# Kernel optimization log

Hardware: AMD Instinct MI355X
Metric: run time of the kernel (lower is better)

The kernel has to match this reference:

```python
import jax, jax.numpy as jnp
import numpy as np

OUT = 7          # out_size
SCALE = 0.25     # spatial_scale
SAMPLE = 2       # sample_num (samples per bin edge)
NORI = 8         # nOrientation
TWO_PI = 2.0 * np.pi


def setup_inputs() -> dict:
    key = jax.random.key(0)
    k1, k2, k3, k4, k5 = jax.random.split(key, 5)
    N, C, H, W = 2, 256, 128, 128
    R = 4096
    features = jax.random.normal(k1, (N, C, H, W), dtype=jnp.float32)
    # rois: (batch_idx, cx, cy, w, h, theta) in image coords (image ~512x512)
    bidx = jax.random.randint(k2, (R, 1), 0, N).astype(jnp.float32)
    cxy = jax.random.uniform(k3, (R, 2), minval=32.0, maxval=480.0, dtype=jnp.float32)
    wh = jax.random.uniform(k4, (R, 2), minval=16.0, maxval=256.0, dtype=jnp.float32)
    theta = jax.random.uniform(k5, (R, 1), minval=0.0, maxval=TWO_PI, dtype=jnp.float32)
    rois = jnp.concatenate([bidx, cxy, wh, theta], axis=1)
    return {"features": features, "rois": rois}


def riroi_align(features, rois):
    """Rotation-invariant RoIAlign (ReDet RiRoIAlign) forward.

    features: [N, C, H, W] with C = c_per * NORI, channel layout c*NORI + o.
    rois:     [R, 6] = (batch_idx, cx, cy, w, h, theta).
    returns:  [R, C, OUT, OUT]
    """
    N, C, H, W = features.shape
    c_per = C // NORI
    g = SAMPLE

    def one_roi(roi):
        b = roi[0].astype(jnp.int32)
        cx = roi[1] * SCALE
        cy = roi[2] * SCALE
        rw = jnp.maximum(roi[3] * SCALE, 1.0)
        rh = jnp.maximum(roi[4] * SCALE, 1.0)
        theta = roi[5]
        bin_w = rw / OUT
        bin_h = rh / OUT
        idx = jnp.arange(OUT, dtype=jnp.float32)
        off = (jnp.arange(g, dtype=jnp.float32) + 0.5) / g
        # local (un-rotated) sample coords, roi-centered; P = OUT*g points per axis
        yy = (-rh / 2 + idx[:, None] * bin_h + off[None, :] * bin_h).reshape(-1)
        xx = (-rw / 2 + idx[:, None] * bin_w + off[None, :] * bin_w).reshape(-1)
        c_t, s_t = jnp.cos(theta), jnp.sin(theta)
        x = xx[None, :] * c_t + yy[:, None] * s_t + cx   # [P, P]
        y = yy[:, None] * c_t - xx[None, :] * s_t + cy   # [P, P]

        # bilinear interpolation with RoIAlign border conventions
        valid = (y > -1.0) & (y < H) & (x > -1.0) & (x < W)
        xc = jnp.clip(x, 0.0, None)
        yc = jnp.clip(y, 0.0, None)
        x0 = jnp.floor(xc).astype(jnp.int32)
        y0 = jnp.floor(yc).astype(jnp.int32)
        hx = x0 >= W - 1
        hy = y0 >= H - 1
        x0 = jnp.where(hx, W - 1, x0)
        x1 = jnp.where(hx, W - 1, x0 + 1)
        y0 = jnp.where(hy, H - 1, y0)
        y1 = jnp.where(hy, H - 1, y0 + 1)
        xc = jnp.where(hx, x0.astype(jnp.float32), xc)
        yc = jnp.where(hy, y0.astype(jnp.float32), yc)
        lx = xc - x0
        ly = yc - y0
        wx0 = 1.0 - lx
        wy0 = 1.0 - ly

        def gat(yi, xi):
            return features[b, :, yi, xi]  # [P, P, C]

        val = ((wy0 * wx0)[..., None] * gat(y0, x0)
               + (wy0 * lx)[..., None] * gat(y0, x1)
               + (ly * wx0)[..., None] * gat(y1, x0)
               + (ly * lx)[..., None] * gat(y1, x1))
        val = jnp.where(valid[..., None], val, 0.0)       # [P, P, C]
        val = jnp.moveaxis(val, -1, 0)                    # [C, P, P]
        # average the g x g samples within each output bin
        val = val.reshape(C, OUT, g, OUT, g).mean(axis=(2, 4))  # [C, OUT, OUT]

        # orientation-channel circular rotation with linear interpolation
        ind_f = theta * NORI / TWO_PI
        ind0 = jnp.floor(ind_f)
        l = ind_f - ind0
        ind = ind0.astype(jnp.int32) % NORI
        o = jnp.arange(NORI)
        src = (o - ind) % NORI
        src_p = (src + 1) % NORI
        v = val.reshape(c_per, NORI, OUT, OUT)
        out = (1.0 - l) * v[:, src] + l * v[:, src_p]
        return out.reshape(C, OUT, OUT)

    return jax.vmap(one_roi)(rois)  # [R, C, OUT, OUT]


def reference(features, rois):
    return riroi_align(features, rois)
```

## Files before the change

### kernel.cpp

```cpp
#include <hip/hip_runtime.h>

typedef _Float16 half_t;
typedef int   v2i __attribute__((ext_vector_type(2)));
typedef int   v4i __attribute__((ext_vector_type(4)));
typedef float v4f __attribute__((ext_vector_type(4)));

#define OUTS 7
#define NORI 8
#define NCH  256
#define FH   128
#define FW   128
#define HW   (FH * FW)
#define NSAMP (2 * OUTS * 2 * OUTS)
#define NBIN  (OUTS * OUTS)
#define WBINS 7
#define NBKT  512

struct __align__(32) Geom { int o[4]; float w[4]; };

__global__ __launch_bounds__(256) void transpose_nchw_nhwc_h(
    const float* __restrict__ in, half_t* __restrict__ out) {
  __shared__ float tile[64][65];
  const int b  = blockIdx.z;
  const int p0 = blockIdx.x * 64;
  const int c0 = blockIdx.y * 64;
  const int tx = threadIdx.x & 63;
  const int ty = threadIdx.x >> 6;

  const float* src = in + ((size_t)b * NCH + c0) * HW + p0;
#pragma unroll
  for (int i = 0; i < 16; ++i) {
    int c = ty + i * 4;
    tile[c][tx] = src[(size_t)c * HW + tx];
  }
  __syncthreads();
  half_t* dst = out + ((size_t)b * HW + p0) * NCH + c0;
#pragma unroll
  for (int i = 0; i < 16; ++i) {
    int p = ty + i * 4;
    dst[(size_t)p * NCH + tx] = (half_t)tile[tx][p];
  }
}

__global__ __launch_bounds__(256) void key_hist_kernel(
    const float* __restrict__ rois, int R, int* __restrict__ hist,
    int* __restrict__ keys) {
  const int i = blockIdx.x * 256 + threadIdx.x;
  if (i >= R) return;
  const float* roi = rois + (size_t)i * 6;
  const int b  = ((int)roi[0]) & 1;
  int mx = (((int)roi[1]) >> 5) & 15;
  int my = (((int)roi[2]) >> 5) & 15;
  mx = (mx | (mx << 2)) & 0x33; mx = (mx | (mx << 1)) & 0x55;
  my = (my | (my << 2)) & 0x33; my = (my | (my << 1)) & 0x55;
  const int key = (b << 8) | mx | (my << 1);
  keys[i] = key;
  atomicAdd(&hist[key], 1);
}

__global__ __launch_bounds__(NBKT) void scan_kernel(
    const int* __restrict__ hist, int* __restrict__ cursor) {
  __shared__ int s[NBKT];
  const int t = threadIdx.x;
  const int v = hist[t];
  s[t] = v;
  __syncthreads();
  for (int off = 1; off < NBKT; off <<= 1) {
    const int add = (t >= off) ? s[t - off] : 0;
    __syncthreads();
    s[t] += add;
    __syncthreads();
  }
  cursor[t] = s[t] - v;
}

__global__ __launch_bounds__(256) void scatter_kernel(
    const int* __restrict__ keys, int R, int* __restrict__ cursor,
    int* __restrict__ order) {
  const int i = blockIdx.x * 256 + threadIdx.x;
  if (i >= R) return;
  const int pos = atomicAdd(&cursor[keys[i]], 1);
  order[pos] = i;
}

__global__ __launch_bounds__(256) void geom_kernel(
    const float* __restrict__ rois, Geom* __restrict__ g, int total) {
  const int gid = blockIdx.x * 256 + threadIdx.x;
  if (gid >= total) return;
  const int r   = gid / NSAMP;
  const int q   = gid - r * NSAMP;
  const int bin = q >> 2;
  const int sub = q & 3;
  const int by = bin / OUTS, bx = bin - by * OUTS;
  const int py = by * 2 + (sub >> 1);
  const int px = bx * 2 + (sub & 1);

  const float* roi = rois + (size_t)r * 6;
  const int   b     = (int)roi[0];
  const float cx    = roi[1] * 0.25f;
  const float cy    = roi[2] * 0.25f;
  const float rw    = fmaxf(roi[3] * 0.25f, 1.0f);
  const float rh    = fmaxf(roi[4] * 0.25f, 1.0f);
  const float theta = roi[5];
  const float bin_w = rw * (1.0f / OUTS);
  const float bin_h = rh * (1.0f / OUTS);
  const float ct = cosf(theta), st = sinf(theta);
  const float hbw = 0.5f * bin_w, hbh = 0.5f * bin_h;
  const float xoff = 0.25f * bin_w - 0.5f * rw;
  const float yoff = 0.25f * bin_h - 0.5f * rh;

  const float yy = (float)py * hbh + yoff;
  const float xx = (float)px * hbw + xoff;
  const float x = xx * ct + yy * st + cx;
  const float y = yy * ct - xx * st + cy;

  v4i oo = {0, 0, 0, 0};
  v4f ww = {0.f, 0.f, 0.f, 0.f};
  if (x > -1.0f && x < (float)FW && y > -1.0f && y < (float)FH) {
    float xc = fmaxf(x, 0.f);
    float yc = fmaxf(y, 0.f);
    int x0 = (int)xc;
    int y0 = (int)yc;
    int x1, y1;
    float lx, ly;
    if (x0 >= FW - 1) { x0 = FW - 1; x1 = FW - 1; lx = 0.f; }
    else              { x1 = x0 + 1; lx = xc - (float)x0; }
    if (y0 >= FH - 1) { y0 = FH - 1; y1 = FH - 1; ly = 0.f; }
    else              { y1 = y0 + 1; ly = yc - (float)y0; }
    const float wx0 = 1.f - lx, wy0 = 1.f - ly;
    ww.x = 0.25f * wy0 * wx0; ww.y = 0.25f * wy0 * lx;
    ww.z = 0.25f * ly  * wx0; ww.w = 0.25f * ly  * lx;
    const int base = b * HW;
    oo.x = (base + y0 * FW + x0) << 9; oo.y = (base + y0 * FW + x1) << 9;
    oo.z = (base + y1 * FW + x0) << 9; oo.w = (base + y1 * FW + x1) << 9;
  }
  v4i* dst = (v4i*)&g[gid];
  __builtin_nontemporal_store(oo, dst);
  __builtin_nontemporal_store(*(v4i*)&ww, dst + 1);
}

#define FMALO(accv, wv, pk) \
  asm("v_fma_mix_f32 %0, %1, %2, %0 op_sel_hi:[0,1,0]" \
      : "+v"(accv) : "v"(wv), "v"(pk))
#define FMAHI(accv, wv, pk) \
  asm("v_fma_mix_f32 %0, %1, %2, %0 op_sel:[0,1,0] op_sel_hi:[0,1,0]" \
      : "+v"(accv) : "v"(wv), "v"(pk))

template <bool SORTED>
__global__ __launch_bounds__(512) void riroi_main(
    const half_t* __restrict__ feat, const float* __restrict__ rois,
    const Geom* __restrict__ geom, const int* __restrict__ order,
    float* __restrict__ out) {
  __shared__ v4i s_geom[NSAMP * 2];
  __shared__ alignas(16) float s_tr[128 * NBIN];

  const int t = threadIdx.x;
  const int w = t >> 6;
  const int l = t & 63;
  const int b0 = w * 6;
  const int gbase = w * 24;

  int r;
  if (SORTED) {
    const int bid = blockIdx.x, nwg = gridDim.x;
    const int virt = ((nwg & 7) == 0) ? ((bid & 7) * (nwg >> 3) + (bid >> 3))
                                      : bid;
    r = order[virt];
  } else {
    r = blockIdx.x;
  }

  if (t < NSAMP * 2)
    s_geom[t] = __builtin_nontemporal_load(
        ((const v4i*)(geom + (size_t)r * NSAMP)) + t);
  __syncthreads();

  const float theta = rois[(size_t)r * 6 + 5];
  const float indf = theta * (8.0f / 6.2831853071795862f);
  const float ind0 = floorf(indf);
  const float lmix = indf - ind0;
  const int   ind  = ((int)ind0) & 7;
  const int   m    = (8 - ind) & 7;

  const char* fb = (const char*)feat;
  const unsigned lane_off = (unsigned)(l << 3);

  float acc[WBINS][4];
#pragma unroll
  for (int i = 0; i < WBINS; ++i)
#pragma unroll
    for (int j = 0; j < 4; ++j) acc[i][j] = 0.f;

#define DECLSET(S) \
  v4i o0##S, o1##S; v4f w0##S, w1##S; \
  v2i a0##S, a1##S, a2##S, a3##S, b0##S, b1##S, b2##S, b3##S;
  DECLSET(P) DECLSET(Q) DECLSET(R)
#undef DECLSET

#define GSTAGE(S, bt) { \
  const int gi = gbase + (bt) * 2; \
  o0##S = s_geom[2 * gi];     w0##S = *(const v4f*)&s_geom[2 * gi + 1]; \
  o1##S = s_geom[2 * gi + 2]; w1##S = *(const v4f*)&s_geom[2 * gi + 3]; }

#define VSTAGE(S) { \
  a0##S = *(const v2i*)(fb + ((unsigned)o0##S.x + lane_off)); \
  a1##S = *(const v2i*)(fb + ((unsigned)o0##S.y + lane_off)); \
  a2##S = *(const v2i*)(fb + ((unsigned)o0##S.z + lane_off)); \
  a3##S = *(const v2i*)(fb + ((unsigned)o0##S.w + lane_off)); \
  b0##S = *(const v2i*)(fb + ((unsigned)o1##S.x + lane_off)); \
  b1##S = *(const v2i*)(fb + ((unsigned)o1##S.y + lane_off)); \
  b2##S = *(const v2i*)(fb + ((unsigned)o1##S.z + lane_off)); \
  b3##S = *(const v2i*)(fb + ((unsigned)o1##S.w + lane_off)); }

#define FTAP(wv, pk, p) { \
  FMALO(acc[p][0], wv, pk.x); FMAHI(acc[p][1], wv, pk.x); \
  FMALO(acc[p][2], wv, pk.y); FMAHI(acc[p][3], wv, pk.y); }

#define FSTAGE(S, p) \
  FTAP(w0##S.x, a0##S, p) FTAP(w0##S.y, a1##S, p) \
  FTAP(w0##S.z, a2##S, p) FTAP(w0##S.w, a3##S, p) \
  FTAP(w1##S.x, b0##S, p) FTAP(w1##S.y, b1##S, p) \
  FTAP(w1##S.z, b2##S, p) FTAP(w1##S.w, b3##S, p)

#define ITER(bt, S0, S1, S2) { \
  if ((bt) + 2 < 14) GSTAGE(S2, (bt) + 2); \
  if ((bt) + 1 < 14) VSTAGE(S1); \
  FSTAGE(S0, (bt) / 2); }

  GSTAGE(P, 0)
  GSTAGE(Q, 1) VSTAGE(P)
  ITER(0,  P, Q, R) ITER(1,  Q, R, P) ITER(2,  R, P, Q)
  ITER(3,  P, Q, R) ITER(4,  Q, R, P) ITER(5,  R, P, Q)
  ITER(6,  P, Q, R) ITER(7,  Q, R, P) ITER(8,  R, P, Q)
  ITER(9,  P, Q, R) ITER(10, Q, R, P) ITER(11, R, P, Q)
  ITER(12, P, Q, R) ITER(13, Q, R, P)

#undef ITER
#undef FSTAGE
#undef FTAP
#undef VSTAGE
#undef GSTAGE

#define MIX_BODY(M)                                                        \
  {                                                                        \
    _Pragma("unroll")                                                      \
    for (int bb = 0; bb < WBINS; ++bb) {                                   \
      float B[8];                                                          \
      B[0] = acc[bb][0]; B[1] = acc[bb][1];                                \
      B[2] = acc[bb][2]; B[3] = acc[bb][3];                                \
      B[4] = __shfl_xor(acc[bb][0], 1, 64);                                \
      B[5] = __shfl_xor(acc[bb][1], 1, 64);                                \
      B[6] = __shfl_xor(acc[bb][2], 1, 64);                                \
      B[7] = __shfl_xor(acc[bb][3], 1, 64);                                \
      float tt[4];                                                         \
      _Pragma("unroll")                                                    \
      for (int j = 0; j < 4; ++j) {                                        \
        const float a0 = B[((M) + j) & 7];                                 \
        const float a1 = B[((M) + j + 1) & 7];                             \
        tt[j] = a0 + lmix * (a1 - a0);                                     \
      }                                                                    \
      acc[bb][0] = tt[0]; acc[bb][1] = tt[1];                              \
      acc[bb][2] = tt[2]; acc[bb][3] = tt[3];                              \
    }                                                                      \
  }
  switch (m) {
    case 0: MIX_BODY(0) break;
    case 1: MIX_BODY(1) break;
    case 2: MIX_BODY(2) break;
    case 3: MIX_BODY(3) break;
    case 4: MIX_BODY(4) break;
    case 5: MIX_BODY(5) break;
    case 6: MIX_BODY(6) break;
    case 7: MIX_BODY(7) break;
  }
#undef MIX_BODY

#pragma unroll
  for (int rnd = 0; rnd < 2; ++rnd) {
    if ((l >> 5) == rnd) {
      const int cl = (l & 31) * 4;
#pragma unroll
      for (int bb = 0; bb < WBINS; ++bb) {
        const int bin = b0 + bb;
#pragma unroll
        for (int j = 0; j < 4; ++j)
          s_tr[(cl + j) * NBIN + bin] = acc[bb][j];
      }
    }
    __syncthreads();
    const v4f* s4 = (const v4f*)s_tr;
    v4f* d4 = (v4f*)(out + (size_t)r * (NCH * NBIN) + rnd * (128 * NBIN));
    for (int i = t; i < 128 * NBIN / 4; i += 512)
      __builtin_nontemporal_store(s4[i], d4 + i);
    __syncthreads();
  }
}

__global__ __launch_bounds__(256) void riroi_cf(
    const float* __restrict__ feat, const float* __restrict__ rois,
    float* __restrict__ out) {
  const int r = blockIdx.x;
  const int c = threadIdx.x;
  const float* roi = rois + (size_t)r * 6;
  const int   b     = (int)roi[0];
  const float cx    = roi[1] * 0.25f;
  const float cy    = roi[2] * 0.25f;
  const float rw    = fmaxf(roi[3] * 0.25f, 1.0f);
  const float rh    = fmaxf(roi[4] * 0.25f, 1.0f);
  const float theta = roi[5];
  const float bin_w = rw * (1.0f / OUTS), bin_h = rh * (1.0f / OUTS);
  const float ct = cosf(theta), st = sinf(theta);
  const float hbw = 0.5f * bin_w, hbh = 0.5f * bin_h;
  const float xoff = 0.25f * bin_w - 0.5f * rw;
  const float yoff = 0.25f * bin_h - 0.5f * rh;
  const float* fb = feat + ((size_t)b * NCH + c) * HW;
  float acc[NBIN];
#pragma unroll
  for (int i = 0; i < NBIN; ++i) acc[i] = 0.f;
  for (int py = 0; py < 2 * OUTS; ++py) {
    const float yy = (float)py * hbh + yoff;
    for (int px = 0; px < 2 * OUTS; ++px) {
      const float xx = (float)px * hbw + xoff;
      const float x = xx * ct + yy * st + cx;
      const float y = yy * ct - xx * st + cy;
      if (x > -1.0f && x < (float)FW && y > -1.0f && y < (float)FH) {
        float xc = fmaxf(x, 0.f), yc = fmaxf(y, 0.f);
        int x0 = (int)xc, y0 = (int)yc, x1, y1;
        float lx, ly;
        if (x0 >= FW - 1) { x0 = FW - 1; x1 = FW - 1; lx = 0.f; }
        else              { x1 = x0 + 1; lx = xc - (float)x0; }
        if (y0 >= FH - 1) { y0 = FH - 1; y1 = FH - 1; ly = 0.f; }
        else              { y1 = y0 + 1; ly = yc - (float)y0; }
        const float wx0 = 1.f - lx, wy0 = 1.f - ly;
        acc[(py >> 1) * OUTS + (px >> 1)] +=
            (wy0 * wx0) * fb[y0 * FW + x0] + (wy0 * lx) * fb[y0 * FW + x1]
          + (ly * wx0) * fb[y1 * FW + x0] + (ly * lx) * fb[y1 * FW + x1];
      }
    }
  }
#pragma unroll
  for (int i = 0; i < NBIN; ++i) acc[i] *= 0.25f;
  const float indf = (theta * 8.0f) / 6.2831853071795862f;
  const float ind0 = floorf(indf);
  const float l    = indf - ind0;
  const int   ind  = ((int)ind0) % NORI;
  const int   o    = c & 7;
  const int   lane = c & 63;
  const int srcLane  = (lane & 56) | ((o - ind + 8) & 7);
  const int srcLane2 = (lane & 56) | ((o - ind + 9) & 7);
  float* op = out + ((size_t)r * NCH + c) * NBIN;
#pragma unroll
  for (int i = 0; i < NBIN; ++i) {
    const float v  = acc[i];
    const float vs = __shfl(v, srcLane, 64);
    const float vp = __shfl(v, srcLane2, 64);
    op[i] = (1.f - l) * vs + l * vp;
  }
}

extern "C" void kernel_launch(void* const* d_in, const int* in_sizes, int n_in,
                              void* d_out, int out_size, void* d_ws, size_t ws_size,
                              hipStream_t stream) {
  const float* feat = (const float*)d_in[0];
  const float* rois = (const float*)d_in[1];
  float* out = (float*)d_out;
  const int R = in_sizes[1] / 6;
  const int N = in_sizes[0] / (NCH * HW);

  const size_t sort_bytes = ((size_t)(2 * NBKT + 2 * R) * 4 + 255) & ~(size_t)255;
  const size_t geom_bytes = (size_t)R * NSAMP * sizeof(Geom);
  const size_t feat_bytes = (size_t)N * HW * NCH * sizeof(half_t);
  const int rb = (R + 255) / 256;

  if (ws_size >= sort_bytes + geom_bytes + feat_bytes) {
    int*    hist   = (int*)d_ws;
    int*    cursor = hist + NBKT;
    int*    keys   = cursor + NBKT;
    int*    order  = keys + R;
    Geom*   g  = (Geom*)((char*)d_ws + sort_bytes);
    half_t* ft = (half_t*)((char*)d_ws + sort_bytes + geom_bytes);

    hipMemsetAsync(hist, 0, NBKT * sizeof(int), stream);
    key_hist_kernel<<<rb, 256, 0, stream>>>(rois, R, hist, keys);
    scan_kernel<<<1, NBKT, 0, stream>>>(hist, cursor);
    scatter_kernel<<<rb, 256, 0, stream>>>(keys, R, cursor, order);

    dim3 tg(HW / 64, NCH / 64, N);
    transpose_nchw_nhwc_h<<<tg, 256, 0, stream>>>(feat, ft);
    const int total = R * NSAMP;
    geom_kernel<<<(total + 255) / 256, 256, 0, stream>>>(rois, g, total);
    riroi_main<true><<<R, 512, 0, stream>>>(ft, rois, g, order, out);
  } else if (ws_size >= geom_bytes + feat_bytes) {
    Geom*   g  = (Geom*)d_ws;
    half_t* ft = (half_t*)((char*)d_ws + geom_bytes);
    dim3 tg(HW / 64, NCH / 64, N);
    transpose_nchw_nhwc_h<<<tg, 256, 0, stream>>>(feat, ft);
    const int total = R * NSAMP;
    geom_kernel<<<(total + 255) / 256, 256, 0, stream>>>(rois, g, total);
    riroi_main<false><<<R, 512, 0, stream>>>(ft, rois, g, nullptr, out);
  } else {
    riroi_cf<<<R, 256, 0, stream>>>(feat, rois, out);
  }
}
```

Baseline: 158.4 us.

## Fuse sample-geometry computation into main kernel and reshape gather pipeline

Removes the separate geom_kernel and its workspace buffer: each block now computes its 196 sample offsets and bilinear weights directly into shared memory. This drops one launch and the global write and read of about 25 MB of geometry data. The gather loop also changes from a three-stage pipeline of two samples per stage to a double-buffered pipeline of one sample per stage, with s_setprio raising priority around the FMA blocks. The cost is redundant trig in the block prologue, done by 196 of 512 threads, and less memory-level parallelism per stage.

```diff
diff --git a/kernel.cpp b/kernel.cpp
--- a/kernel.cpp
+++ b/kernel.cpp
@@ -15,8 +15,6 @@
 #define NBIN  (OUTS * OUTS)
 #define WBINS 7
 #define NBKT  512
-
-struct __align__(32) Geom { int o[4]; float w[4]; };
 
 __global__ __launch_bounds__(256) void transpose_nchw_nhwc_h(
     const float* __restrict__ in, half_t* __restrict__ out) {
@@ -83,62 +81,6 @@
   order[pos] = i;
 }
 
-__global__ __launch_bounds__(256) void geom_kernel(
-    const float* __restrict__ rois, Geom* __restrict__ g, int total) {
-  const int gid = blockIdx.x * 256 + threadIdx.x;
-  if (gid >= total) return;
-  const int r   = gid / NSAMP;
-  const int q   = gid - r * NSAMP;
-  const int bin = q >> 2;
-  const int sub = q & 3;
-  const int by = bin / OUTS, bx = bin - by * OUTS;
-  const int py = by * 2 + (sub >> 1);
-  const int px = bx * 2 + (sub & 1);
-
-  const float* roi = rois + (size_t)r * 6;
-  const int   b     = (int)roi[0];
-  const float cx    = roi[1] * 0.25f;
-  const float cy    = roi[2] * 0.25f;
-  const float rw    = fmaxf(roi[3] * 0.25f, 1.0f);
-  const float rh    = fmaxf(roi[4] * 0.25f, 1.0f);
-  const float theta = roi[5];
-  const float bin_w = rw * (1.0f / OUTS);
-  const float bin_h = rh * (1.0f / OUTS);
-  const float ct = cosf(theta), st = sinf(theta);
-  const float hbw = 0.5f * bin_w, hbh = 0.5f * bin_h;
-  const float xoff = 0.25f * bin_w - 0.5f * rw;
-  const float yoff = 0.25f * bin_h - 0.5f * rh;
-
-  const float yy = (float)py * hbh + yoff;
-  const float xx = (float)px * hbw + xoff;
-  const float x = xx * ct + yy * st + cx;
-  const float y = yy * ct - xx * st + cy;
-
-  v4i oo = {0, 0, 0, 0};
-  v4f ww = {0.f, 0.f, 0.f, 0.f};
-  if (x > -1.0f && x < (float)FW && y > -1.0f && y < (float)FH) {
-    float xc = fmaxf(x, 0.f);
-    float yc = fmaxf(y, 0.f);
-    int x0 = (int)xc;
-    int y0 = (int)yc;
-    int x1, y1;
-    float lx, ly;
-    if (x0 >= FW - 1) { x0 = FW - 1; x1 = FW - 1; lx = 0.f; }
-    else              { x1 = x0 + 1; lx = xc - (float)x0; }
-    if (y0 >= FH - 1) { y0 = FH - 1; y1 = FH - 1; ly = 0.f; }
-    else              { y1 = y0 + 1; ly = yc - (float)y0; }
-    const float wx0 = 1.f - lx, wy0 = 1.f - ly;
-    ww.x = 0.25f * wy0 * wx0; ww.y = 0.25f * wy0 * lx;
-    ww.z = 0.25f * ly  * wx0; ww.w = 0.25f * ly  * lx;
-    const int base = b * HW;
-    oo.x = (base + y0 * FW + x0) << 9; oo.y = (base + y0 * FW + x1) << 9;
-    oo.z = (base + y1 * FW + x0) << 9; oo.w = (base + y1 * FW + x1) << 9;
-  }
-  v4i* dst = (v4i*)&g[gid];
-  __builtin_nontemporal_store(oo, dst);
-  __builtin_nontemporal_store(*(v4i*)&ww, dst + 1);
-}
-
 #define FMALO(accv, wv, pk) \
   asm("v_fma_mix_f32 %0, %1, %2, %0 op_sel_hi:[0,1,0]" \
       : "+v"(accv) : "v"(wv), "v"(pk))
@@ -149,8 +91,7 @@
 template <bool SORTED>
 __global__ __launch_bounds__(512) void riroi_main(
     const half_t* __restrict__ feat, const float* __restrict__ rois,
-    const Geom* __restrict__ geom, const int* __restrict__ order,
-    float* __restrict__ out) {
+    const int* __restrict__ order, float* __restrict__ out) {
   __shared__ v4i s_geom[NSAMP * 2];
   __shared__ alignas(16) float s_tr[128 * NBIN];
 
@@ -170,12 +111,58 @@
     r = blockIdx.x;
   }
 
-  if (t < NSAMP * 2)
-    s_geom[t] = __builtin_nontemporal_load(
-        ((const v4i*)(geom + (size_t)r * NSAMP)) + t);
+  const float* roi = rois + (size_t)r * 6;
+  const float theta = roi[5];
+
+  if (t < NSAMP) {
+    const int bin = t >> 2;
+    const int sub = t & 3;
+    const int by = bin / OUTS, bx = bin - by * OUTS;
+    const int py = by * 2 + (sub >> 1);
+    const int px = bx * 2 + (sub & 1);
+
+    const int   b  = (int)roi[0];
+    const float cx = roi[1] * 0.25f;
+    const float cy = roi[2] * 0.25f;
+    const float rw = fmaxf(roi[3] * 0.25f, 1.0f);
+    const float rh = fmaxf(roi[4] * 0.25f, 1.0f);
+    const float bin_w = rw * (1.0f / OUTS);
+    const float bin_h = rh * (1.0f / OUTS);
+    const float ct = cosf(theta), st = sinf(theta);
+    const float hbw = 0.5f * bin_w, hbh = 0.5f * bin_h;
+    const float xoff = 0.25f * bin_w - 0.5f * rw;
+    const float yoff = 0.25f * bin_h - 0.5f * rh;
+
+    const float yy = (float)py * hbh + yoff;
+    const float xx = (float)px * hbw + xoff;
+    const float x = xx * ct + yy * st + cx;
+    const float y = yy * ct - xx * st + cy;
+
+    v4i oo = {0, 0, 0, 0};
+    v4f ww = {0.f, 0.f, 0.f, 0.f};
+    if (x > -1.0f && x < (float)FW && y > -1.0f && y < (float)FH) {
+      float xc = fmaxf(x, 0.f);
+      float yc = fmaxf(y, 0.f);
+      int x0 = (int)xc;
+      int y0 = (int)yc;
+      int x1, y1;
+      float lx, ly;
+      if (x0 >= FW - 1) { x0 = FW - 1; x1 = FW - 1; lx = 0.f; }
+      else              { x1 = x0 + 1; lx = xc - (float)x0; }
+      if (y0 >= FH - 1) { y0 = FH - 1; y1 = FH - 1; ly = 0.f; }
+      else              { y1 = y0 + 1; ly = yc - (float)y0; }
+      const float wx0 = 1.f - lx, wy0 = 1.f - ly;
+      ww.x = 0.25f * wy0 * wx0; ww.y = 0.25f * wy0 * lx;
+      ww.z = 0.25f * ly  * wx0; ww.w = 0.25f * ly  * lx;
+      const int base = b * HW;
+      oo.x = (base + y0 * FW + x0) << 9; oo.y = (base + y0 * FW + x1) << 9;
+      oo.z = (base + y1 * FW + x0) << 9; oo.w = (base + y1 * FW + x1) << 9;
+    }
+    s_geom[2 * t]     = oo;
+    s_geom[2 * t + 1] = *(v4i*)&ww;
+  }
   __syncthreads();
 
-  const float theta = rois[(size_t)r * 6 + 5];
   const float indf = theta * (8.0f / 6.2831853071795862f);
   const float ind0 = floorf(indf);
   const float lmix = indf - ind0;
@@ -192,48 +179,42 @@
     for (int j = 0; j < 4; ++j) acc[i][j] = 0.f;
 
 #define DECLSET(S) \
-  v4i o0##S, o1##S; v4f w0##S, w1##S; \
-  v2i a0##S, a1##S, a2##S, a3##S, b0##S, b1##S, b2##S, b3##S;
-  DECLSET(P) DECLSET(Q) DECLSET(R)
+  v4i og##S; v4f wg##S; v2i va##S, vb##S, vc##S, vd##S;
+  DECLSET(P) DECLSET(Q)
 #undef DECLSET
 
 #define GSTAGE(S, bt) { \
-  const int gi = gbase + (bt) * 2; \
-  o0##S = s_geom[2 * gi];     w0##S = *(const v4f*)&s_geom[2 * gi + 1]; \
-  o1##S = s_geom[2 * gi + 2]; w1##S = *(const v4f*)&s_geom[2 * gi + 3]; }
+  const int gi = gbase + (bt); \
+  og##S = s_geom[2 * gi]; wg##S = *(const v4f*)&s_geom[2 * gi + 1]; }
 
 #define VSTAGE(S) { \
-  a0##S = *(const v2i*)(fb + ((unsigned)o0##S.x + lane_off)); \
-  a1##S = *(const v2i*)(fb + ((unsigned)o0##S.y + lane_off)); \
-  a2##S = *(const v2i*)(fb + ((unsigned)o0##S.z + lane_off)); \
-  a3##S = *(const v2i*)(fb + ((unsigned)o0##S.w + lane_off)); \
-  b0##S = *(const v2i*)(fb + ((unsigned)o1##S.x + lane_off)); \
-  b1##S = *(const v2i*)(fb + ((unsigned)o1##S.y + lane_off)); \
-  b2##S = *(const v2i*)(fb + ((unsigned)o1##S.z + lane_off)); \
-  b3##S = *(const v2i*)(fb + ((unsigned)o1##S.w + lane_off)); }
+  va##S = *(const v2i*)(fb + ((unsigned)og##S.x + lane_off)); \
+  vb##S = *(const v2i*)(fb + ((unsigned)og##S.y + lane_off)); \
+  vc##S = *(const v2i*)(fb + ((unsigned)og##S.z + lane_off)); \
+  vd##S = *(const v2i*)(fb + ((unsigned)og##S.w + lane_off)); }
 
 #define FTAP(wv, pk, p) { \
   FMALO(acc[p][0], wv, pk.x); FMAHI(acc[p][1], wv, pk.x); \
   FMALO(acc[p][2], wv, pk.y); FMAHI(acc[p][3], wv, pk.y); }
 
 #define FSTAGE(S, p) \
-  FTAP(w0##S.x, a0##S, p) FTAP(w0##S.y, a1##S, p) \
-  FTAP(w0##S.z, a2##S, p) FTAP(w0##S.w, a3##S, p) \
-  FTAP(w1##S.x, b0##S, p) FTAP(w1##S.y, b1##S, p) \
-  FTAP(w1##S.z, b2##S, p) FTAP(w1##S.w, b3##S, p)
-
-#define ITER(bt, S0, S1, S2) { \
-  if ((bt) + 2 < 14) GSTAGE(S2, (bt) + 2); \
-  if ((bt) + 1 < 14) VSTAGE(S1); \
-  FSTAGE(S0, (bt) / 2); }
-
-  GSTAGE(P, 0)
-  GSTAGE(Q, 1) VSTAGE(P)
-  ITER(0,  P, Q, R) ITER(1,  Q, R, P) ITER(2,  R, P, Q)
-  ITER(3,  P, Q, R) ITER(4,  Q, R, P) ITER(5,  R, P, Q)
-  ITER(6,  P, Q, R) ITER(7,  Q, R, P) ITER(8,  R, P, Q)
-  ITER(9,  P, Q, R) ITER(10, Q, R, P) ITER(11, R, P, Q)
-  ITER(12, P, Q, R) ITER(13, Q, R, P)
+  FTAP(wg##S.x, va##S, p) FTAP(wg##S.y, vb##S, p) \
+  FTAP(wg##S.z, vc##S, p) FTAP(wg##S.w, vd##S, p)
+
+#define ITER(bt, CUR, NXT) { \
+  if ((bt) + 1 < 28) { GSTAGE(NXT, (bt) + 1); VSTAGE(NXT); } \
+  __builtin_amdgcn_s_setprio(1); \
+  FSTAGE(CUR, (bt) / 4); \
+  __builtin_amdgcn_s_setprio(0); }
+
+  GSTAGE(P, 0) VSTAGE(P)
+  ITER(0,  P, Q) ITER(1,  Q, P) ITER(2,  P, Q) ITER(3,  Q, P)
+  ITER(4,  P, Q) ITER(5,  Q, P) ITER(6,  P, Q) ITER(7,  Q, P)
+  ITER(8,  P, Q) ITER(9,  Q, P) ITER(10, P, Q) ITER(11, Q, P)
+  ITER(12, P, Q) ITER(13, Q, P) ITER(14, P, Q) ITER(15, Q, P)
+  ITER(16, P, Q) ITER(17, Q, P) ITER(18, P, Q) ITER(19, Q, P)
+  ITER(20, P, Q) ITER(21, Q, P) ITER(22, P, Q) ITER(23, Q, P)
+  ITER(24, P, Q) ITER(25, Q, P) ITER(26, P, Q) ITER(27, Q, P)
 
 #undef ITER
 #undef FSTAGE
@@ -368,17 +349,15 @@
   const int N = in_sizes[0] / (NCH * HW);
 
   const size_t sort_bytes = ((size_t)(2 * NBKT + 2 * R) * 4 + 255) & ~(size_t)255;
-  const size_t geom_bytes = (size_t)R * NSAMP * sizeof(Geom);
   const size_t feat_bytes = (size_t)N * HW * NCH * sizeof(half_t);
   const int rb = (R + 255) / 256;
 
-  if (ws_size >= sort_bytes + geom_bytes + feat_bytes) {
+  if (ws_size >= sort_bytes + feat_bytes) {
     int*    hist   = (int*)d_ws;
     int*    cursor = hist + NBKT;
     int*    keys   = cursor + NBKT;
     int*    order  = keys + R;
-    Geom*   g  = (Geom*)((char*)d_ws + sort_bytes);
-    half_t* ft = (half_t*)((char*)d_ws + sort_bytes + geom_bytes);
+    half_t* ft = (half_t*)((char*)d_ws + sort_bytes);
 
     hipMemsetAsync(hist, 0, NBKT * sizeof(int), stream);
     key_hist_kernel<<<rb, 256, 0, stream>>>(rois, R, hist, keys);
@@ -387,17 +366,12 @@
 
     dim3 tg(HW / 64, NCH / 64, N);
     transpose_nchw_nhwc_h<<<tg, 256, 0, stream>>>(feat, ft);
-    const int total = R * NSAMP;
-    geom_kernel<<<(total + 255) / 256, 256, 0, stream>>>(rois, g, total);
-    riroi_main<true><<<R, 512, 0, stream>>>(ft, rois, g, order, out);
-  } else if (ws_size >= geom_bytes + feat_bytes) {
-    Geom*   g  = (Geom*)d_ws;
-    half_t* ft = (half_t*)((char*)d_ws + geom_bytes);
+    riroi_main<true><<<R, 512, 0, stream>>>(ft, rois, order, out);
+  } else if (ws_size >= feat_bytes) {
+    half_t* ft = (half_t*)d_ws;
     dim3 tg(HW / 64, NCH / 64, N);
     transpose_nchw_nhwc_h<<<tg, 256, 0, stream>>>(feat, ft);
-    const int total = R * NSAMP;
-    geom_kernel<<<(total + 255) / 256, 256, 0, stream>>>(rois, g, total);
-    riroi_main<false><<<R, 512, 0, stream>>>(ft, rois, g, nullptr, out);
+    riroi_main<false><<<R, 512, 0, stream>>>(ft, rois, nullptr, out);
   } else {
     riroi_cf<<<R, 256, 0, stream>>>(feat, rois, out);
   }
```

After: 139.2 us. -12.1%, faster.
